# Kernel tuning notes

Hardware: AMD Instinct MI355X
Metric: run time of the kernel (lower is better)

The kernel has to match this reference:

```python
import jax, jax.numpy as jnp
from jax import lax
import numpy as np

B, N, C = 8, 4096, 64
NPOINT = 1024
RADII = (0.1, 0.2, 0.4)
NSAMPLES = (16, 32, 128)
MLPS = ((32, 32, 64), (64, 64, 128), (64, 96, 128))


def setup_inputs() -> dict:
    key = jax.random.key(0)
    ks = jax.random.split(key, 32)
    inp = {
        "xyz": jax.random.uniform(ks[0], (B, N, 3), jnp.float32),
        "points": jax.random.normal(ks[1], (B, N, C), jnp.float32),
    }
    k = 2
    for bi, widths in enumerate(MLPS):
        cin = C + 3  # use_xyz concatenates relative coords
        for li, cout in enumerate(widths):
            inp[f"w{bi}_{li}"] = jax.random.normal(ks[k], (cin, cout), jnp.float32) * (1.0 / np.sqrt(cin))
            k += 1
            inp[f"b{bi}_{li}"] = jnp.zeros((cout,), jnp.float32)
            cin = cout
    return inp


def farthest_point_sample(xyz, npoint):
    # xyz: [B,N,3] -> idx [B,npoint] int32. Deterministic start at point 0.
    Bb, Nn, _ = xyz.shape

    def step(carry, _):
        dists, farthest = carry  # [B,N], [B]
        centroid = jnp.take_along_axis(xyz, farthest[:, None, None], axis=1)  # [B,1,3]
        d = jnp.sum((xyz - centroid) ** 2, axis=-1)
        dists = jnp.minimum(dists, d)
        return (dists, jnp.argmax(dists, axis=-1).astype(jnp.int32)), farthest

    init = (jnp.full((Bb, Nn), 1e10, xyz.dtype), jnp.zeros((Bb,), jnp.int32))
    _, idx = lax.scan(step, init, None, length=npoint)
    return jnp.transpose(idx)  # [B, npoint]


def _ball_query(d2, radius, nsample, Nn):
    # d2: [B,S,N] squared distances. First nsample indices (in original order)
    # within radius; empty slots filled with the first valid index (center
    # point is always within its own ball, so a valid index always exists).
    key = jnp.where(d2 < radius * radius, jnp.arange(Nn, dtype=jnp.int32), Nn)
    srt = jnp.sort(key, axis=-1)[..., :nsample]  # [B,S,nsample]
    first = srt[..., :1]
    return jnp.where(srt == Nn, first, srt)


def _group(x, idx):
    # x: [B,N,D], idx: [B,S,K] -> [B,S,K,D]
    return jax.vmap(lambda p, i: p[i])(x, idx)


def _forward(xyz, points, params):
    Nn = xyz.shape[1]
    fps_idx = farthest_point_sample(xyz, NPOINT)                 # [B,S]
    new_xyz = jnp.take_along_axis(xyz, fps_idx[..., None], axis=1)  # [B,S,3]
    d2 = jnp.sum((new_xyz[:, :, None, :] - xyz[:, None, :, :]) ** 2, axis=-1)  # [B,S,N]
    outs = []
    for r, ns, layers in zip(RADII, NSAMPLES, params):
        idx = _ball_query(d2, r, ns, Nn)                          # [B,S,ns]
        g_xyz = _group(xyz, idx) - new_xyz[:, :, None, :]         # [B,S,ns,3]
        g = jnp.concatenate([_group(points, idx), g_xyz], axis=-1)  # [B,S,ns,C+3]
        for w, b in layers:  # 1x1 Conv2d == per-neighbor dense + relu
            g = jax.nn.relu(g @ w + b)
        outs.append(jnp.max(g, axis=2))                           # [B,S,cout]
    return new_xyz, jnp.concatenate(outs, axis=-1)


def reference(xyz, points,
              w0_0, b0_0, w0_1, b0_1, w0_2, b0_2,
              w1_0, b1_0, w1_1, b1_1, w1_2, b1_2,
              w2_0, b2_0, w2_1, b2_1, w2_2, b2_2):
    params = [
        [(w0_0, b0_0), (w0_1, b0_1), (w0_2, b0_2)],
        [(w1_0, b1_0), (w1_1, b1_1), (w1_2, b1_2)],
        [(w2_0, b2_0), (w2_1, b2_1), (w2_2, b2_2)],
    ]
    return _forward(xyz, points, params)
```

## Files before the change

kernel.cpp:

```cpp
#include <hip/hip_runtime.h>
#include <hip/hip_bf16.h>
#include <stdint.h>

typedef unsigned long long u64;
typedef __attribute__((ext_vector_type(8))) short bf16x8;
typedef __attribute__((ext_vector_type(4))) float f32x4;
typedef __attribute__((ext_vector_type(2))) float f32x2;

#define SCOPE_AGENT __HIP_MEMORY_SCOPE_AGENT

__device__ __forceinline__ unsigned short f2bf(float f) {
    unsigned x = __float_as_uint(f);
    unsigned r = (x + 0x7fffu + ((x >> 16) & 1u)) >> 16;
    return (unsigned short)r;
}

__device__ __forceinline__ bf16x8 cvt8(float4 a, float4 b) {
    union { bf16x8 v; __hip_bfloat162 h[4]; } u;
    u.h[0] = __float22bfloat162_rn({a.x, a.y});
    u.h[1] = __float22bfloat162_rn({a.z, a.w});
    u.h[2] = __float22bfloat162_rn({b.x, b.y});
    u.h[3] = __float22bfloat162_rn({b.z, b.w});
    return u.v;
}

__device__ __forceinline__ float wave_max_dpp(float v) {
#define DPP_MAX_STEP(ctrl)                                                     \
    v = fmaxf(v, __int_as_float(__builtin_amdgcn_update_dpp(                   \
               0, __float_as_int(v), (ctrl), 0xf, 0xf, true)))
    DPP_MAX_STEP(0xB1);
    DPP_MAX_STEP(0x4E);
    DPP_MAX_STEP(0x141);
    DPP_MAX_STEP(0x140);
    DPP_MAX_STEP(0x142);
    DPP_MAX_STEP(0x143);
#undef DPP_MAX_STEP
    return __int_as_float(__builtin_amdgcn_readlane(__float_as_int(v), 63));
}

struct WPack { const float* w[9]; const float* b[9]; };

__device__ __forceinline__ void fps_path(const float* __restrict__ xyz,
                                         float* __restrict__ newxyz,
                                         unsigned* __restrict__ flags,
                                         unsigned char* smem) {
#pragma clang fp contract(off)
    __builtin_amdgcn_s_setprio(3);
    float* xs = (float*)smem;
    float* ys = xs + 4096;
    float* zs = ys + 4096;
    u64* skey = (u64*)(smem + 49152);

    const int b = blockIdx.x;
    const int t = threadIdx.x;
    const int lane = t & 63;
    const int wave = t >> 6;

    f32x2 px[8], py[8], pz[8], dist[8];
    {
        union { float4 v[12]; float f[48]; } u;
        const float4* src =
            reinterpret_cast<const float4*>(xyz + (size_t)b * 12288) + t * 12;
#pragma unroll
        for (int w = 0; w < 12; ++w) u.v[w] = src[w];
#pragma unroll
        for (int i = 0; i < 8; ++i) {
            px[i] = (f32x2){u.f[6 * i + 0], u.f[6 * i + 3]};
            py[i] = (f32x2){u.f[6 * i + 1], u.f[6 * i + 4]};
            pz[i] = (f32x2){u.f[6 * i + 2], u.f[6 * i + 5]};
            dist[i] = (f32x2){1e10f, 1e10f};
            const int j = t * 16 + 2 * i;
            xs[j] = px[i].x; xs[j + 1] = px[i].y;
            ys[j] = py[i].x; ys[j + 1] = py[i].y;
            zs[j] = pz[i].x; zs[j + 1] = pz[i].y;
        }
    }
    __syncthreads();

    int far = 0;
    for (int k = 0; k < 1024; ++k) {
        const float cx = xs[far], cy = ys[far], cz = zs[far];
        if (t == 0) {
            const size_t o = ((size_t)b * 1024 + k) * 3;
            __hip_atomic_store(&newxyz[o + 0], cx, __ATOMIC_RELAXED, SCOPE_AGENT);
            __hip_atomic_store(&newxyz[o + 1], cy, __ATOMIC_RELAXED, SCOPE_AGENT);
            __hip_atomic_store(&newxyz[o + 2], cz, __ATOMIC_RELAXED, SCOPE_AGENT);
            if ((k & 15) == 15) {
                asm volatile("s_waitcnt vmcnt(0)" ::: "memory");
                __hip_atomic_store(&flags[b * 16], (unsigned)(k + 1),
                                   __ATOMIC_RELAXED, SCOPE_AGENT);
            }
        }
        const f32x2 c2x = (f32x2){cx, cx};
        const f32x2 c2y = (f32x2){cy, cy};
        const f32x2 c2z = (f32x2){cz, cz};
#pragma unroll
        for (int i = 0; i < 8; ++i) {
            const f32x2 dx = px[i] - c2x;
            const f32x2 dy = py[i] - c2y;
            const f32x2 dz = pz[i] - c2z;
            const f32x2 s = dx * dx + dy * dy;
            const f32x2 d = s + dz * dz;
            dist[i].x = fminf(dist[i].x, d.x);
            dist[i].y = fminf(dist[i].y, d.y);
        }
        float dv[16];
#pragma unroll
        for (int i = 0; i < 8; ++i) { dv[2 * i] = dist[i].x; dv[2 * i + 1] = dist[i].y; }
        float m8[8], m4[4], bv;
#pragma unroll
        for (int i = 0; i < 8; ++i) m8[i] = fmaxf(dv[i], dv[i + 8]);
#pragma unroll
        for (int i = 0; i < 4; ++i) m4[i] = fmaxf(m8[i], m8[i + 4]);
        bv = fmaxf(fmaxf(m4[0], m4[1]), fmaxf(m4[2], m4[3]));
        int bj = 15;
#pragma unroll
        for (int i = 14; i >= 0; --i) bj = (dv[i] == bv) ? i : bj;
        const int myidx = t * 16 + bj;

        const float wmax = wave_max_dpp(bv);
        const u64 mask = __ballot(bv == wmax);
        const int fl = (int)__builtin_ctzll(mask);
        const int widx = __builtin_amdgcn_readlane(myidx, fl);

        const int pp = k & 1;
        if (lane == 0)
            skey[pp * 4 + wave] =
                ((u64)__float_as_uint(wmax) << 32) | (unsigned)(4095 - widx);
        __syncthreads();
        const ulonglong2 ka = *reinterpret_cast<const ulonglong2*>(&skey[pp * 4 + 0]);
        const ulonglong2 kb = *reinterpret_cast<const ulonglong2*>(&skey[pp * 4 + 2]);
        const u64 m01 = (ka.x > ka.y) ? ka.x : ka.y;
        const u64 m23 = (kb.x > kb.y) ? kb.x : kb.y;
        const u64 mm = (m01 > m23) ? m01 : m23;
        far = 4095 - (int)(unsigned)(mm & 0xffffffffull);
    }
}

__device__ __forceinline__ void prep_path(const WPack& p,
                                          unsigned short* __restrict__ wout,
                                          float* __restrict__ bout,
                                          unsigned* __restrict__ flags) {
    constexpr int cin[9]  = {67, 32, 32,  67, 64, 64,  67, 64, 96};
    constexpr int cout[9] = {32, 32, 64,  64, 64, 128, 64, 96, 128};
    constexpr int sw[9]   = {104, 40, 40, 104, 72, 72, 104, 72, 104};
    constexpr int woff[9] = {0, 3328, 4608, 7168, 13824, 18432, 27648, 34304, 41216};
    constexpr int boff[9] = {0, 32, 64, 128, 192, 256, 384, 448, 544};
    const int L = blockIdx.x - 8;
    const float* w = p.w[L];
    const int ci = cin[L], co = cout[L], s = sw[L];
    unsigned short* dst = wout + woff[L];
    for (int e = threadIdx.x; e < co * s; e += 256) {
        const int n = e / s, k = e % s;
        dst[e] = (k < ci) ? f2bf(w[(size_t)k * co + n]) : (unsigned short)0;
    }
    for (int e = threadIdx.x; e < co; e += 256) bout[boff[L] + e] = p.b[L][e];
    __syncthreads();
    if (threadIdx.x == 0)
        __hip_atomic_fetch_add(&flags[128], 1u, __ATOMIC_RELEASE, SCOPE_AGENT);
}

template <int NS>
__device__ __forceinline__ void ballq1(const float* __restrict__ base,
                                       float cx, float cy, float cz, float r2,
                                       unsigned short* __restrict__ out, int lane) {
    int cnt = 0, first = 0;
    const u64 lower = (((u64)1) << lane) - 1;
    for (int it = 0; it < 64; ++it) {
        const int j = it * 64 + lane;
        const float* pp = base + j * 3;
        const float dx = pp[0] - cx;
        const float dy = pp[1] - cy;
        const float dz = pp[2] - cz;
        const float d2 = __fadd_rn(__fadd_rn(__fmul_rn(dx, dx), __fmul_rn(dy, dy)),
                                   __fmul_rn(dz, dz));
        const bool in = d2 < r2;
        const u64 m = __ballot(in);
        if (cnt == 0 && m) first = it * 64 + (int)__builtin_ctzll(m);
        const int pos = cnt + (int)__builtin_popcountll(m & lower);
        if (in && pos < NS) out[pos] = (unsigned short)j;
        cnt += (int)__builtin_popcountll(m);
        if (cnt >= NS) break;
    }
    for (int pos = cnt + lane; pos < NS; pos += 64) out[pos] = (unsigned short)first;
}

template <int MW, int Cout, int SOUT>
__device__ __forceinline__ void layer1_direct(
    const float* __restrict__ pts,
    const float* __restrict__ xyzb,
    const unsigned short* __restrict__ idxb,
    float ncx, float ncy, float ncz,
    const unsigned short* __restrict__ Wg, const float* __restrict__ bg,
    unsigned short* __restrict__ dst, int lane, int mslice) {
    constexpr int SW = 104;
    constexpr int MT = MW / 16;
    constexpr int NT = Cout / 16;
    const int ml = lane & 15;
    const int quad = lane >> 4;

    bf16x8 afr[MT][3];
#pragma unroll
    for (int mt = 0; mt < MT; ++mt) {
        const int row = mslice * MW + mt * 16 + ml;
        const int id = idxb[row] & 4095;
        const float* rb = pts + ((size_t)id << 6) + quad * 8;
        const float4* r4 = reinterpret_cast<const float4*>(rb);
        afr[mt][0] = cvt8(r4[0], r4[1]);
        const float4* r4b = reinterpret_cast<const float4*>(rb + 32);
        afr[mt][1] = cvt8(r4b[0], r4b[1]);
        union { bf16x8 v; unsigned short h[8]; } tg;
        tg.v = (bf16x8)(short)0;
        if (quad == 0) {
            const float* pz = xyzb + (size_t)id * 3;
            tg.h[0] = f2bf(pz[0] - ncx);
            tg.h[1] = f2bf(pz[1] - ncy);
            tg.h[2] = f2bf(pz[2] - ncz);
        }
        afr[mt][2] = tg.v;
    }

    f32x4 acc[MT][NT];
#pragma unroll
    for (int mt = 0; mt < MT; ++mt)
#pragma unroll
        for (int nt = 0; nt < NT; ++nt) acc[mt][nt] = (f32x4){0.f, 0.f, 0.f, 0.f};

#pragma unroll
    for (int ks = 0; ks < 3; ++ks) {
        bf16x8 bfr[NT];
#pragma unroll
        for (int nt = 0; nt < NT; ++nt)
            bfr[nt] = *reinterpret_cast<const bf16x8*>(
                Wg + (nt * 16 + ml) * SW + ks * 32 + quad * 8);
#pragma unroll
        for (int mt = 0; mt < MT; ++mt)
#pragma unroll
            for (int nt = 0; nt < NT; ++nt)
                acc[mt][nt] = __builtin_amdgcn_mfma_f32_16x16x32_bf16(
                    afr[mt][ks], bfr[nt], acc[mt][nt], 0, 0, 0);
    }

#pragma unroll
    for (int nt = 0; nt < NT; ++nt) {
        const int col = nt * 16 + ml;
        const float bv = bg[col];
#pragma unroll
        for (int mt = 0; mt < MT; ++mt)
#pragma unroll
            for (int r = 0; r < 4; ++r) {
                const float v = fmaxf(acc[mt][nt][r] + bv, 0.0f);
                dst[(mslice * MW + mt * 16 + quad * 4 + r) * SOUT + col] = f2bf(v);
            }
    }
}

template <int MW, int Kp, int Cout, int SIN>
__device__ __forceinline__ void layer_mid(const unsigned short* __restrict__ src,
                                          unsigned short* __restrict__ dst,
                                          const unsigned short* __restrict__ Wg,
                                          const float* __restrict__ bg,
                                          int lane, int mslice) {
    constexpr int MT = MW / 16;
    constexpr int NT = Cout / 16;
    constexpr int SOUT = Cout + 8;
    const int ml = lane & 15;
    const int quad = lane >> 4;

    f32x4 acc[MT][NT];
#pragma unroll
    for (int mt = 0; mt < MT; ++mt)
#pragma unroll
        for (int nt = 0; nt < NT; ++nt) acc[mt][nt] = (f32x4){0.f, 0.f, 0.f, 0.f};

#pragma unroll
    for (int ks = 0; ks < Kp; ks += 32) {
        bf16x8 afr[MT], bfr[NT];
#pragma unroll
        for (int mt = 0; mt < MT; ++mt)
            afr[mt] = *reinterpret_cast<const bf16x8*>(
                src + (mslice * MW + mt * 16 + ml) * SIN + ks + quad * 8);
#pragma unroll
        for (int nt = 0; nt < NT; ++nt)
            bfr[nt] = *reinterpret_cast<const bf16x8*>(
                Wg + (nt * 16 + ml) * SIN + ks + quad * 8);
#pragma unroll
        for (int mt = 0; mt < MT; ++mt)
#pragma unroll
            for (int nt = 0; nt < NT; ++nt)
                acc[mt][nt] = __builtin_amdgcn_mfma_f32_16x16x32_bf16(
                    afr[mt], bfr[nt], acc[mt][nt], 0, 0, 0);
    }

#pragma unroll
    for (int nt = 0; nt < NT; ++nt) {
        const int col = nt * 16 + ml;
        const float bv = bg[col];
#pragma unroll
        for (int mt = 0; mt < MT; ++mt)
#pragma unroll
            for (int r = 0; r < 4; ++r) {
                const float v = fmaxf(acc[mt][nt][r] + bv, 0.0f);
                dst[(mslice * MW + mt * 16 + quad * 4 + r) * SOUT + col] = f2bf(v);
            }
    }
}

template <int MW, int Kp, int Cout, int SIN, bool DIRECT>
__device__ __forceinline__ void layer_last(const unsigned short* __restrict__ src,
                                           const unsigned short* __restrict__ Wg,
                                           const float* __restrict__ bg,
                                           float* __restrict__ out,
                                           int lane, int mslice) {
    constexpr int MT = MW / 16;
    constexpr int NT = Cout / 16;
    const int ml = lane & 15;
    const int quad = lane >> 4;

    f32x4 acc[MT][NT];
#pragma unroll
    for (int mt = 0; mt < MT; ++mt)
#pragma unroll
        for (int nt = 0; nt < NT; ++nt) acc[mt][nt] = (f32x4){0.f, 0.f, 0.f, 0.f};

#pragma unroll
    for (int ks = 0; ks < Kp; ks += 32) {
        bf16x8 afr[MT], bfr[NT];
#pragma unroll
        for (int mt = 0; mt < MT; ++mt)
            afr[mt] = *reinterpret_cast<const bf16x8*>(
                src + (mslice * MW + mt * 16 + ml) * SIN + ks + quad * 8);
#pragma unroll
        for (int nt = 0; nt < NT; ++nt)
            bfr[nt] = *reinterpret_cast<const bf16x8*>(
                Wg + (nt * 16 + ml) * SIN + ks + quad * 8);
#pragma unroll
        for (int mt = 0; mt < MT; ++mt)
#pragma unroll
            for (int nt = 0; nt < NT; ++nt)
                acc[mt][nt] = __builtin_amdgcn_mfma_f32_16x16x32_bf16(
                    afr[mt], bfr[nt], acc[mt][nt], 0, 0, 0);
    }

#pragma unroll
    for (int nt = 0; nt < NT; ++nt) {
        const int col = nt * 16 + ml;
        const float bv = bg[col];
        float mx = 0.0f;
#pragma unroll
        for (int mt = 0; mt < MT; ++mt)
#pragma unroll
            for (int r = 0; r < 4; ++r) mx = fmaxf(mx, acc[mt][nt][r] + bv);
        mx = fmaxf(mx, __shfl_xor(mx, 16, 64));
        mx = fmaxf(mx, __shfl_xor(mx, 32, 64));
        if (quad == 0) {
            if constexpr (DIRECT) out[col] = mx;
            else atomicMax(reinterpret_cast<int*>(out + col), __float_as_int(mx));
        }
    }
}

template <int NS, int C1, int C2, int C3, int CH_OFF>
__device__ __forceinline__ void consume_small(
    unsigned char* smem, const float* __restrict__ xyz,
    const float* __restrict__ points, const float* __restrict__ newxyz,
    const unsigned short* wg1, const unsigned short* wg2, const unsigned short* wg3,
    const float* bg1, const float* bg2, const float* bg3,
    float* __restrict__ outfeat, int gbase, int bb, float r2) {
    constexpr int SB = C1 + 8, SC = C2 + 8;
    unsigned short* Bb = (unsigned short*)smem;
    unsigned short* Cb = Bb + 4 * NS * SB;
    unsigned short* idxb = Cb + 4 * NS * SC;
    const int lane = threadIdx.x & 63;
    const int wave = threadIdx.x >> 6;
    const int g = gbase + wave;
    const float* nc = newxyz + (size_t)g * 3;
    const float ncx = nc[0], ncy = nc[1], ncz = nc[2];
    const float* xb = xyz + (size_t)bb * 12288;
    unsigned short* idxw = idxb + wave * NS;
    ballq1<NS>(xb, ncx, ncy, ncz, r2, idxw, lane);
    layer1_direct<NS, C1, SB>(points + ((size_t)bb << 18), xb, idxw, ncx, ncy, ncz,
                              wg1, bg1, Bb + wave * NS * SB, lane, 0);
    layer_mid<NS, C1, C2, SB>(Bb + wave * NS * SB, Cb + wave * NS * SC, wg2, bg2,
                              lane, 0);
    layer_last<NS, C2, C3, SC, true>(Cb + wave * NS * SC, wg3, bg3,
                                     outfeat + (size_t)g * 320 + CH_OFF, lane, 0);
}

__device__ __forceinline__ void consume_b3(
    unsigned char* smem, const float* __restrict__ xyz,
    const float* __restrict__ points, const float* __restrict__ newxyz,
    const unsigned short* wg1, const unsigned short* wg2, const unsigned short* wg3,
    const float* bg1, const float* bg2, const float* bg3,
    float* __restrict__ outfeat, int g, int bb) {
    constexpr int SB = 72, SC = 104;
    unsigned short* Bb = (unsigned short*)smem;
    unsigned short* Cb = Bb + 128 * SB;
    float* Mx = (float*)(Cb + 128 * SC);
    unsigned short* idxb = (unsigned short*)(Mx + 128);
    const int tid = threadIdx.x;
    const int lane = tid & 63;
    const int wave = tid >> 6;
    const float* nc = newxyz + (size_t)g * 3;
    const float ncx = nc[0], ncy = nc[1], ncz = nc[2];
    const float* xb = xyz + (size_t)bb * 12288;
    if (wave == 0) ballq1<128>(xb, ncx, ncy, ncz, 0.16f, idxb, lane);
    if (tid >= 128) Mx[tid - 128] = 0.0f;
    __syncthreads();
    layer1_direct<32, 64, SB>(points + ((size_t)bb << 18), xb, idxb, ncx, ncy, ncz,
                              wg1, bg1, Bb, lane, wave);
    layer_mid<32, 64, 96, SB>(Bb, Cb, wg2, bg2, lane, wave);
    layer_last<32, 96, 128, SC, false>(Cb, wg3, bg3, Mx, lane, wave);
    __syncthreads();
    if (tid < 128) outfeat[(size_t)g * 320 + 192 + tid] = Mx[tid];
}

__global__ __launch_bounds__(256, 3) void mega_kernel(
    const float* __restrict__ xyz, const float* __restrict__ points, WPack p,
    float* __restrict__ newxyz, float* __restrict__ outfeat,
    unsigned* __restrict__ flags, unsigned short* __restrict__ wprep,
    float* __restrict__ bprep) {
    __shared__ __align__(16) unsigned char smem[49280];
    const int bx = blockIdx.x;
    if (bx < 8) { fps_path(xyz, newxyz, flags, smem); return; }
    if (bx < 17) prep_path(p, wprep, bprep, flags);

    if (threadIdx.x == 0) {
        while (__hip_atomic_load(&flags[128], __ATOMIC_RELAXED, SCOPE_AGENT) < 9u)
            __builtin_amdgcn_s_sleep(8);
        (void)__hip_atomic_load(&flags[128], __ATOMIC_ACQUIRE, SCOPE_AGENT);
    }
    __syncthreads();

    for (int item = bx - 8; item < 12288; item += 760) {
        const int chunk = item / 48;
        const int r = item - chunk * 48;
        int bb, br, soff = 0;
        if (r < 8)       { br = 0; bb = r; }
        else if (r < 16) { br = 1; bb = r - 8; }
        else             { br = 2; bb = (r - 16) & 7; soff = (r - 16) >> 3; }
        const unsigned need = (unsigned)(chunk * 4 + 4);
        if (threadIdx.x == 0) {
            const unsigned* pf = &flags[bb * 16];
            while (__hip_atomic_load(pf, __ATOMIC_RELAXED, SCOPE_AGENT) < need)
                __builtin_amdgcn_s_sleep(2);
            (void)__hip_atomic_load(pf, __ATOMIC_ACQUIRE, SCOPE_AGENT);
        }
        __syncthreads();
        const int gbase = bb * 1024 + chunk * 4;
        if (br == 0)
            consume_small<16, 32, 32, 64, 0>(smem, xyz, points, newxyz,
                wprep + 0, wprep + 3328, wprep + 4608,
                bprep + 0, bprep + 32, bprep + 64, outfeat, gbase, bb, 0.01f);
        else if (br == 1)
            consume_small<32, 64, 64, 128, 64>(smem, xyz, points, newxyz,
                wprep + 7168, wprep + 13824, wprep + 18432,
                bprep + 128, bprep + 192, bprep + 256, outfeat, gbase, bb, 0.04f);
        else
            consume_b3(smem, xyz, points, newxyz,
                wprep + 27648, wprep + 34304, wprep + 41216,
                bprep + 384, bprep + 448, bprep + 544, outfeat, gbase + soff, bb);
    }
}

extern "C" void kernel_launch(void* const* d_in, const int* in_sizes, int n_in,
                              void* d_out, int out_size, void* d_ws, size_t ws_size,
                              hipStream_t stream) {
    (void)in_sizes; (void)n_in; (void)out_size; (void)ws_size;
    const float* xyz = (const float*)d_in[0];
    const float* points = (const float*)d_in[1];
    WPack pack;
    int p = 2;
    for (int L = 0; L < 9; ++L) {
        pack.w[L] = (const float*)d_in[p++];
        pack.b[L] = (const float*)d_in[p++];
    }
    float* newxyz = (float*)d_out;
    float* outfeat = (float*)d_out + 8 * 1024 * 3;

    unsigned* flags = (unsigned*)d_ws;
    unsigned short* wprep = (unsigned short*)((char*)d_ws + 1024);
    float* bprep = (float*)((char*)d_ws + 1024 + 109056);

    hipMemsetAsync(d_ws, 0, 1024, stream);
    mega_kernel<<<dim3(768), dim3(256), 0, stream>>>(
        xyz, points, pack, newxyz, outfeat, flags, wprep, bprep);
}
```

Baseline: 686.2 us.

## Replace per-batch FPS flags with poison polling, dynamic work queue, CU-aware dozing

The output centroid buffer is pre-filled with a poison pattern, and consumer waves poll each centroid directly instead of waiting on per-16-step batch flags. Static item striding is replaced by a global atomic work counter. Consumer blocks co-resident on the same CU as an FPS block, identified through hardware registers, sleep until FPS finishes so they do not steal issue slots from the serial FPS loop. This adds an extra memset and more polling traffic, and it relies on the poison value never being a legitimate coordinate.

```diff
diff --git a/kernel.cpp b/kernel.cpp
--- a/kernel.cpp
+++ b/kernel.cpp
@@ -8,6 +8,13 @@
 typedef __attribute__((ext_vector_type(2))) float f32x2;
 
 #define SCOPE_AGENT __HIP_MEMORY_SCOPE_AGENT
+#define POISON 0xFFFFFFFFu
+
+#define H_ITEM 0
+#define H_PREP 1
+#define H_PLACED 2
+#define H_FDONE 3
+#define H_SLEEP 4
 
 __device__ __forceinline__ unsigned short f2bf(float f) {
     unsigned x = __float_as_uint(f);
@@ -38,11 +45,18 @@
     return __int_as_float(__builtin_amdgcn_readlane(__float_as_int(v), 63));
 }
 
+__device__ __forceinline__ unsigned cu_key() {
+    unsigned hw = (unsigned)__builtin_amdgcn_s_getreg(14852) & 0xffu;
+    unsigned xcc = (unsigned)__builtin_amdgcn_s_getreg(6164) & 0x7u;
+    return (xcc << 8) | hw;
+}
+
 struct WPack { const float* w[9]; const float* b[9]; };
 
 __device__ __forceinline__ void fps_path(const float* __restrict__ xyz,
                                          float* __restrict__ newxyz,
-                                         unsigned* __restrict__ flags,
+                                         unsigned* __restrict__ hdr,
+                                         unsigned* __restrict__ occ,
                                          unsigned char* smem) {
 #pragma clang fp contract(off)
     __builtin_amdgcn_s_setprio(3);
@@ -55,6 +69,11 @@
     const int t = threadIdx.x;
     const int lane = t & 63;
     const int wave = t >> 6;
+
+    if (t == 0) {
+        __hip_atomic_store(&occ[cu_key()], 1u, __ATOMIC_RELAXED, SCOPE_AGENT);
+        __hip_atomic_fetch_add(&hdr[H_PLACED], 1u, __ATOMIC_RELEASE, SCOPE_AGENT);
+    }
 
     f32x2 px[8], py[8], pz[8], dist[8];
     {
@@ -85,11 +104,6 @@
             __hip_atomic_store(&newxyz[o + 0], cx, __ATOMIC_RELAXED, SCOPE_AGENT);
             __hip_atomic_store(&newxyz[o + 1], cy, __ATOMIC_RELAXED, SCOPE_AGENT);
             __hip_atomic_store(&newxyz[o + 2], cz, __ATOMIC_RELAXED, SCOPE_AGENT);
-            if ((k & 15) == 15) {
-                asm volatile("s_waitcnt vmcnt(0)" ::: "memory");
-                __hip_atomic_store(&flags[b * 16], (unsigned)(k + 1),
-                                   __ATOMIC_RELAXED, SCOPE_AGENT);
-            }
         }
         const f32x2 c2x = (f32x2){cx, cx};
         const f32x2 c2y = (f32x2){cy, cy};
@@ -135,12 +149,14 @@
         const u64 mm = (m01 > m23) ? m01 : m23;
         far = 4095 - (int)(unsigned)(mm & 0xffffffffull);
     }
+    if (t == 0)
+        __hip_atomic_fetch_add(&hdr[H_FDONE], 1u, __ATOMIC_RELEASE, SCOPE_AGENT);
 }
 
 __device__ __forceinline__ void prep_path(const WPack& p,
                                           unsigned short* __restrict__ wout,
                                           float* __restrict__ bout,
-                                          unsigned* __restrict__ flags) {
+                                          unsigned* __restrict__ hdr) {
     constexpr int cin[9]  = {67, 32, 32,  67, 64, 64,  67, 64, 96};
     constexpr int cout[9] = {32, 32, 64,  64, 64, 128, 64, 96, 128};
     constexpr int sw[9]   = {104, 40, 40, 104, 72, 72, 104, 72, 104};
@@ -157,7 +173,26 @@
     for (int e = threadIdx.x; e < co; e += 256) bout[boff[L] + e] = p.b[L][e];
     __syncthreads();
     if (threadIdx.x == 0)
-        __hip_atomic_fetch_add(&flags[128], 1u, __ATOMIC_RELEASE, SCOPE_AGENT);
+        __hip_atomic_fetch_add(&hdr[H_PREP], 1u, __ATOMIC_RELEASE, SCOPE_AGENT);
+}
+
+__device__ __forceinline__ void poll_centroid(const float* __restrict__ newxyz,
+                                              int g, int lane,
+                                              float& ncx, float& ncy, float& ncz) {
+    const unsigned* ncw = (const unsigned*)(newxyz + (size_t)g * 3);
+    unsigned w0 = 0, w1 = 0, w2 = 0;
+    if (lane == 0) {
+        for (;;) {
+            w0 = __hip_atomic_load(&ncw[0], __ATOMIC_RELAXED, SCOPE_AGENT);
+            w1 = __hip_atomic_load(&ncw[1], __ATOMIC_RELAXED, SCOPE_AGENT);
+            w2 = __hip_atomic_load(&ncw[2], __ATOMIC_RELAXED, SCOPE_AGENT);
+            if (w0 != POISON && w1 != POISON && w2 != POISON) break;
+            __builtin_amdgcn_s_sleep(4);
+        }
+    }
+    ncx = __uint_as_float((unsigned)__builtin_amdgcn_readfirstlane((int)w0));
+    ncy = __uint_as_float((unsigned)__builtin_amdgcn_readfirstlane((int)w1));
+    ncz = __uint_as_float((unsigned)__builtin_amdgcn_readfirstlane((int)w2));
 }
 
 template <int NS>
@@ -374,8 +409,8 @@
     const int lane = threadIdx.x & 63;
     const int wave = threadIdx.x >> 6;
     const int g = gbase + wave;
-    const float* nc = newxyz + (size_t)g * 3;
-    const float ncx = nc[0], ncy = nc[1], ncz = nc[2];
+    float ncx, ncy, ncz;
+    poll_centroid(newxyz, g, lane, ncx, ncy, ncz);
     const float* xb = xyz + (size_t)bb * 12288;
     unsigned short* idxw = idxb + wave * NS;
     ballq1<NS>(xb, ncx, ncy, ncz, r2, idxw, lane);
@@ -398,15 +433,20 @@
     unsigned short* Cb = Bb + 128 * SB;
     float* Mx = (float*)(Cb + 128 * SC);
     unsigned short* idxb = (unsigned short*)(Mx + 128);
+    float* mail = (float*)(idxb + 128);
     const int tid = threadIdx.x;
     const int lane = tid & 63;
     const int wave = tid >> 6;
-    const float* nc = newxyz + (size_t)g * 3;
-    const float ncx = nc[0], ncy = nc[1], ncz = nc[2];
     const float* xb = xyz + (size_t)bb * 12288;
-    if (wave == 0) ballq1<128>(xb, ncx, ncy, ncz, 0.16f, idxb, lane);
+    float ncx, ncy, ncz;
+    if (wave == 0) {
+        poll_centroid(newxyz, g, lane, ncx, ncy, ncz);
+        if (lane == 0) { mail[0] = ncx; mail[1] = ncy; mail[2] = ncz; }
+        ballq1<128>(xb, ncx, ncy, ncz, 0.16f, idxb, lane);
+    }
     if (tid >= 128) Mx[tid - 128] = 0.0f;
     __syncthreads();
+    if (wave != 0) { ncx = mail[0]; ncy = mail[1]; ncz = mail[2]; }
     layer1_direct<32, 64, SB>(points + ((size_t)bb << 18), xb, idxb, ncx, ncy, ncz,
                               wg1, bg1, Bb, lane, wave);
     layer_mid<32, 64, 96, SB>(Bb, Cb, wg2, bg2, lane, wave);
@@ -418,35 +458,46 @@
 __global__ __launch_bounds__(256, 3) void mega_kernel(
     const float* __restrict__ xyz, const float* __restrict__ points, WPack p,
     float* __restrict__ newxyz, float* __restrict__ outfeat,
-    unsigned* __restrict__ flags, unsigned short* __restrict__ wprep,
-    float* __restrict__ bprep) {
+    unsigned* __restrict__ hdr, unsigned* __restrict__ occ,
+    unsigned short* __restrict__ wprep, float* __restrict__ bprep) {
     __shared__ __align__(16) unsigned char smem[49280];
+    __shared__ int itemLDS[2];
     const int bx = blockIdx.x;
-    if (bx < 8) { fps_path(xyz, newxyz, flags, smem); return; }
-    if (bx < 17) prep_path(p, wprep, bprep, flags);
+    if (bx < 8) { fps_path(xyz, newxyz, hdr, occ, smem); return; }
+    if (bx < 17) prep_path(p, wprep, bprep, hdr);
 
     if (threadIdx.x == 0) {
-        while (__hip_atomic_load(&flags[128], __ATOMIC_RELAXED, SCOPE_AGENT) < 9u)
+        while (__hip_atomic_load(&hdr[H_PLACED], __ATOMIC_RELAXED, SCOPE_AGENT) < 8u)
+            __builtin_amdgcn_s_sleep(2);
+        (void)__hip_atomic_load(&hdr[H_PLACED], __ATOMIC_ACQUIRE, SCOPE_AGENT);
+        bool doze = false;
+        if (__hip_atomic_load(&occ[cu_key()], __ATOMIC_RELAXED, SCOPE_AGENT)) {
+            const unsigned prev = __hip_atomic_fetch_add(&hdr[H_SLEEP], 1u,
+                                                         __ATOMIC_RELAXED, SCOPE_AGENT);
+            doze = (prev < 24u);
+        }
+        if (doze)
+            while (__hip_atomic_load(&hdr[H_FDONE], __ATOMIC_RELAXED, SCOPE_AGENT) < 8u)
+                __builtin_amdgcn_s_sleep(127);
+        while (__hip_atomic_load(&hdr[H_PREP], __ATOMIC_RELAXED, SCOPE_AGENT) < 9u)
             __builtin_amdgcn_s_sleep(8);
-        (void)__hip_atomic_load(&flags[128], __ATOMIC_ACQUIRE, SCOPE_AGENT);
-    }
-    __syncthreads();
-
-    for (int item = bx - 8; item < 12288; item += 760) {
+        (void)__hip_atomic_load(&hdr[H_PREP], __ATOMIC_ACQUIRE, SCOPE_AGENT);
+    }
+
+    for (int slot = 0;; slot ^= 1) {
+        if (threadIdx.x == 0)
+            itemLDS[slot] = (int)__hip_atomic_fetch_add(&hdr[H_ITEM], 1u,
+                                                        __ATOMIC_RELAXED, SCOPE_AGENT);
+        __syncthreads();
+        const int item = itemLDS[slot];
+        if (item >= 12288) break;
+
         const int chunk = item / 48;
         const int r = item - chunk * 48;
         int bb, br, soff = 0;
         if (r < 8)       { br = 0; bb = r; }
         else if (r < 16) { br = 1; bb = r - 8; }
         else             { br = 2; bb = (r - 16) & 7; soff = (r - 16) >> 3; }
-        const unsigned need = (unsigned)(chunk * 4 + 4);
-        if (threadIdx.x == 0) {
-            const unsigned* pf = &flags[bb * 16];
-            while (__hip_atomic_load(pf, __ATOMIC_RELAXED, SCOPE_AGENT) < need)
-                __builtin_amdgcn_s_sleep(2);
-            (void)__hip_atomic_load(pf, __ATOMIC_ACQUIRE, SCOPE_AGENT);
-        }
-        __syncthreads();
         const int gbase = bb * 1024 + chunk * 4;
         if (br == 0)
             consume_small<16, 32, 32, 64, 0>(smem, xyz, points, newxyz,
@@ -478,11 +529,13 @@
     float* newxyz = (float*)d_out;
     float* outfeat = (float*)d_out + 8 * 1024 * 3;
 
-    unsigned* flags = (unsigned*)d_ws;
-    unsigned short* wprep = (unsigned short*)((char*)d_ws + 1024);
-    float* bprep = (float*)((char*)d_ws + 1024 + 109056);
-
-    hipMemsetAsync(d_ws, 0, 1024, stream);
+    unsigned* hdr = (unsigned*)d_ws;
+    unsigned* occ = (unsigned*)((char*)d_ws + 256);
+    unsigned short* wprep = (unsigned short*)((char*)d_ws + 8448);
+    float* bprep = (float*)((char*)d_ws + 8448 + 109056);
+
+    hipMemsetAsync(d_ws, 0, 8448, stream);
+    hipMemsetAsync(newxyz, 0xFF, 8 * 1024 * 3 * 4, stream);
     mega_kernel<<<dim3(768), dim3(256), 0, stream>>>(
-        xyz, points, pack, newxyz, outfeat, flags, wprep, bprep);
-}
+        xyz, points, pack, newxyz, outfeat, hdr, occ, wprep, bprep);
+}
```

Measured after the change: 663.8 us. 1.03x faster.
